# Kernel optimization log

Hardware: AMD Instinct MI355X
Metric: run time of the kernel (lower is better)

## Reference

```python
import jax, jax.numpy as jnp
import numpy as np

H = 1024

def gru_step(x, h, W_ih, W_hh, b_ih, b_hh):
    # torch.nn.GRUCell math; gate order r, z, n
    gi = x @ W_ih.T + b_ih            # [N, 3H]
    gh = h @ W_hh.T + b_hh            # [N, 3H]
    i_r, i_z, i_n = jnp.split(gi, 3, axis=-1)
    h_r, h_z, h_n = jnp.split(gh, 3, axis=-1)
    r = jax.nn.sigmoid(i_r + h_r)
    z = jax.nn.sigmoid(i_z + h_z)
    n = jnp.tanh(i_n + r * h_n)
    return (1.0 - z) * n + z * h


def setup_inputs() -> dict:
    key = jax.random.key(0)
    ks = jax.random.split(key, 12)
    V, Nr, Na = 256, 4096, 4096
    s = 1.0 / np.sqrt(H)
    return {
        'state': jax.random.normal(ks[0], (1, H), jnp.float32),
        'rel_tokens': jax.random.randint(ks[1], (Nr, 3), 0, V, jnp.int32),
        'attr_tokens': jax.random.randint(ks[2], (Na, 2), 0, V, jnp.int32),
        'table': jax.random.normal(ks[3], (V, H), jnp.float32),
        'W_emb': jax.random.normal(ks[4], (H, H), jnp.float32) * s,
        'b_emb': jnp.zeros((H,), jnp.float32),
        'W_ih': jax.random.normal(ks[5], (3 * H, H), jnp.float32) * s,
        'W_hh': jax.random.normal(ks[6], (3 * H, H), jnp.float32) * s,
        'b_ih': jnp.zeros((3 * H,), jnp.float32),
        'b_hh': jnp.zeros((3 * H,), jnp.float32),
        'W1': jax.random.normal(ks[7], (H, H), jnp.float32) * s,
        'b1': jnp.zeros((H,), jnp.float32),
        'W2': jax.random.normal(ks[8], (H, H), jnp.float32) * s,
        'b2': jnp.zeros((H,), jnp.float32),
        'W3': jax.random.normal(ks[9], (1, H), jnp.float32) * s,
        'b3': jnp.zeros((1,), jnp.float32),
        'eps': jax.random.uniform(ks[10], (1,), jnp.float32) * 0.1,
    }


def reference(state, rel_tokens, attr_tokens, table, W_emb, b_emb,
              W_ih, W_hh, b_ih, b_hh, W1, b1, W2, b2, W3, b3, eps):
    Nr, Na = rel_tokens.shape[0], attr_tokens.shape[0]
    # per-clause token embeddings passed through embedding_layer (Linear)
    rel_e = jnp.einsum('nte,he->nth', table[rel_tokens], W_emb) + b_emb   # [Nr,3,H]
    att_e = jnp.einsum('nte,he->nth', table[attr_tokens], W_emb) + b_emb  # [Na,2,H]

    # relation clauses: 3 chained GRU steps from global state
    h = jnp.broadcast_to(state, (Nr, H))
    for t in range(3):
        h = gru_step(rel_e[:, t], h, W_ih, W_hh, b_ih, b_hh)
    rel_h = h
    # attribute clauses: 2 chained GRU steps from global state
    h = jnp.broadcast_to(state, (Na, H))
    for t in range(2):
        h = gru_step(att_e[:, t], h, W_ih, W_hh, b_ih, b_hh)
    attr_h = h

    clause = jnp.concatenate([rel_h, attr_h], axis=0)          # [N, H]
    x = jax.nn.relu(clause @ W1.T + b1)
    x = jax.nn.relu(x @ W2.T + b2)
    logits = (x @ W3.T + b3).reshape(1, -1)                    # [1, N]
    probs = jax.nn.softmax(logits, axis=1)                     # softmax over clauses
    n = jnp.float32(probs.shape[1])
    probs = probs * (1.0 - eps[0]) + eps[0] / n                # eps smoothing
    return probs
```

## Files before the change

kernel.cpp:

```cpp
#include <hip/hip_runtime.h>
#include <math.h>

#define H 1024
#define H3 3072
#define NVOC 256

typedef __attribute__((ext_vector_type(8))) short bf16x8;
typedef __attribute__((ext_vector_type(4))) float f32x4;

__device__ __forceinline__ float sigf(float x) { return 1.0f / (1.0f + expf(-x)); }

__device__ __forceinline__ unsigned short f2bf(float f) {
    unsigned int u = __float_as_uint(f);
    u = (u + 0x7fffu + ((u >> 16) & 1u)) >> 16;
    return (unsigned short)u;
}
__device__ __forceinline__ float bf2f(unsigned short u) {
    return __uint_as_float(((unsigned int)u) << 16);
}

#define MM256(MH, AV, BV)                                                          \
    __builtin_amdgcn_s_setprio(1);                                                 \
    _Pragma("unroll")                                                              \
    for (int m_ = 0; m_ < 4; ++m_)                                                 \
        _Pragma("unroll")                                                          \
        for (int n_ = 0; n_ < 4; ++n_)                                             \
            acc[(MH) * 4 + m_][n_] = __builtin_amdgcn_mfma_f32_16x16x32_bf16(      \
                AV[m_], BV[n_], acc[(MH) * 4 + m_][n_], 0, 0, 0);                  \
    __builtin_amdgcn_s_setprio(0);

#define RDA256(BUF, KQ, MH)                                                        \
    _Pragma("unroll")                                                              \
    for (int m_ = 0; m_ < 4; ++m_)                                                 \
        a[m_] = *reinterpret_cast<const bf16x8*>(                                  \
            ldsb + (BUF) * 65536 + ((KQ) * 2 + (MH)) * 8192 + m_ * 1024 + aoff);

#define RDB256(BUF, KQ, DST)                                                       \
    _Pragma("unroll")                                                              \
    for (int n_ = 0; n_ < 4; ++n_)                                                 \
        DST[n_] = *reinterpret_cast<const bf16x8*>(                                \
            ldsb + (BUF) * 65536 + (KQ) * 16384 + n_ * 1024 + boff);

#define BAR256() __builtin_amdgcn_s_barrier()

template<bool RELU, int OUT_MODE>
__global__ __launch_bounds__(512, 2)
void gemm256(const unsigned short* __restrict__ A, const unsigned short* __restrict__ W,
             const float* __restrict__ bias, void* __restrict__ C,
             int N, int K, int gx,
             const float* __restrict__ w3, float* __restrict__ logits)
{
    __shared__ unsigned short lds[65536];
    char* ldsb = (char*)lds;
    const int tid = threadIdx.x;
    const int wid = tid >> 6, lane = tid & 63;

    const int nwg = gridDim.x;
    const int cpx = nwg >> 3;
    const int bid = blockIdx.x;
    const int swz = (bid & 7) * cpx + (bid >> 3);
    const int bm = (swz / gx) * 256;
    const int bn = (swz % gx) * 256;

    const int g = wid >> 2;
    const int wn = (wid & 3) * 64;
    const int fr = lane & 15, fq = lane >> 4;

    const int aoff = (g * 64 + fr) * 64 + ((fq ^ (fr & 3)) * 16);
    const int boff = (wn + fr) * 64 + ((fq ^ (fr & 3)) * 16) + 32768;

    const int srow = tid >> 2;
    const int scol = ((tid & 3) ^ (srow & 3)) * 8;
    const int arow0 = ((srow >> 6) << 7) + (srow & 63);

    auto stageA = [&](int t, int mh) {
        const int buf = t & 1;
        const unsigned short* src = A + (size_t)(bm + arow0 + mh * 64) * K + t * 64 + scol;
#pragma unroll
        for (int kh = 0; kh < 2; ++kh) {
            char* dst = ldsb + buf * 65536 + (kh * 2 + mh) * 8192 + wid * 1024;
            __builtin_amdgcn_global_load_lds(
                (const __attribute__((address_space(1))) void*)(src + kh * 32),
                (__attribute__((address_space(3))) void*)dst, 16, 0, 0);
        }
    };
    auto stageB = [&](int t, int kh) {
        const int buf = t & 1;
        const unsigned short* src = W + (size_t)(bn + srow) * K + t * 64 + kh * 32 + scol;
#pragma unroll
        for (int j = 0; j < 2; ++j) {
            char* dst = ldsb + buf * 65536 + 32768 + kh * 16384 + j * 8192 + wid * 1024;
            __builtin_amdgcn_global_load_lds(
                (const __attribute__((address_space(1))) void*)(src + (size_t)j * 128 * K),
                (__attribute__((address_space(3))) void*)dst, 16, 0, 0);
        }
    };

    f32x4 acc[8][4];
#pragma unroll
    for (int i = 0; i < 8; i++)
#pragma unroll
        for (int j = 0; j < 4; j++) acc[i][j] = (f32x4){0.f, 0.f, 0.f, 0.f};
    bf16x8 a[4], b0[4], b1[4];

    const int nt = K >> 6;
    const int nIter = nt >> 1;

    stageB(0, 0); stageA(0, 0); stageB(0, 1); stageA(0, 1);
    stageB(1, 0); stageA(1, 0); stageB(1, 1);
    asm volatile("s_waitcnt vmcnt(6)" ::: "memory");
    __builtin_amdgcn_sched_barrier(0);
    BAR256();

    for (int it = 0; it < nIter; ++it) {
        const int t0 = 2 * it;
        const bool full = (it + 1 < nIter);
        RDB256(0, 0, b0); RDA256(0, 0, 0);
        stageA(t0 + 1, 1);
        MM256(0, a, b0); BAR256();
        RDB256(0, 1, b1); RDA256(0, 1, 0);
        if (full) stageB(t0 + 2, 0);
        MM256(0, a, b1); BAR256();
        RDA256(0, 0, 1);
        if (full) stageA(t0 + 2, 0);
        MM256(1, a, b0); BAR256();
        RDA256(0, 1, 1);
        if (full) stageB(t0 + 2, 1);
        MM256(1, a, b1);
        if (full) { asm volatile("s_waitcnt vmcnt(6)" ::: "memory"); }
        else      { asm volatile("s_waitcnt vmcnt(0)" ::: "memory"); }
        __builtin_amdgcn_sched_barrier(0);
        BAR256();
        RDB256(1, 0, b0); RDA256(1, 0, 0);
        if (full) stageA(t0 + 2, 1);
        MM256(0, a, b0); BAR256();
        RDB256(1, 1, b1); RDA256(1, 1, 0);
        if (full) stageB(t0 + 3, 0);
        MM256(0, a, b1); BAR256();
        RDA256(1, 0, 1);
        if (full) stageA(t0 + 3, 0);
        MM256(1, a, b0); BAR256();
        RDA256(1, 1, 1);
        if (full) stageB(t0 + 3, 1);
        MM256(1, a, b1);
        if (full) {
            asm volatile("s_waitcnt vmcnt(6)" ::: "memory");
            __builtin_amdgcn_sched_barrier(0);
        }
        BAR256();
    }

    if (OUT_MODE == 2) {
        float rs[8][4];
#pragma unroll
        for (int m = 0; m < 8; m++)
#pragma unroll
            for (int j = 0; j < 4; j++) rs[m][j] = 0.f;
#pragma unroll
        for (int n = 0; n < 4; n++) {
            const int col = bn + wn + n * 16 + fr;
            const float bv = bias[col];
            const float wv = w3[col];
#pragma unroll
            for (int m = 0; m < 8; m++)
#pragma unroll
                for (int j = 0; j < 4; j++) {
                    float v = acc[m][n][j] + bv;
                    if (RELU) v = fmaxf(v, 0.f);
                    rs[m][j] = fmaf(v, wv, rs[m][j]);
                }
        }
#pragma unroll
        for (int m = 0; m < 8; m++)
#pragma unroll
            for (int j = 0; j < 4; j++) {
                float s = rs[m][j];
                s += __shfl_xor(s, 1); s += __shfl_xor(s, 2);
                s += __shfl_xor(s, 4); s += __shfl_xor(s, 8);
                if (fr == 0) {
                    const int row = bm + g * 128 + (m >> 2) * 64 + (m & 3) * 16 + fq * 4 + j;
                    atomicAdd(logits + row, s);
                }
            }
    } else {
#pragma unroll
        for (int m = 0; m < 8; m++) {
#pragma unroll
            for (int n = 0; n < 4; n++) {
                const int col = bn + wn + n * 16 + fr;
                const float bv = bias[col];
#pragma unroll
                for (int j = 0; j < 4; j++) {
                    const int row = bm + g * 128 + (m >> 2) * 64 + (m & 3) * 16 + fq * 4 + j;
                    float v = acc[m][n][j] + bv;
                    if (RELU) v = fmaxf(v, 0.f);
                    ((unsigned short*)C)[(size_t)row * N + col] = f2bf(v);
                }
            }
        }
    }
}

template<bool RELU, int OUT_MODE>
__global__ __launch_bounds__(256)
void gemm_bf16(const unsigned short* __restrict__ A, const unsigned short* __restrict__ W,
               const float* __restrict__ bias, void* __restrict__ C,
               int N, int K, int gx, int Kc,
               const float* __restrict__ w3, float* __restrict__ logits)
{
    __shared__ unsigned short As[4][128 * 32];
    __shared__ unsigned short Ws[4][128 * 32];
    const int tid = threadIdx.x;
    const int wid = tid >> 6, lane = tid & 63;

    const int nwg = gridDim.x;
    const int cpx = nwg >> 3;
    const int bid = blockIdx.x;
    const int swz = (bid & 7) * cpx + (bid >> 3);
    const int bm = (swz / gx) * 128;
    const int bn = (swz % gx) * 128;
    const int k_base = blockIdx.y * Kc;
    const int nt = Kc >> 5;

    const int wm = (wid >> 1) * 64, wn = (wid & 1) * 64;
    const int fr = lane & 15;
    const int fq = lane >> 4;
    const int perm = fq ^ (fr & 3);

    f32x4 acc[4][4];
#pragma unroll
    for (int i = 0; i < 4; i++)
#pragma unroll
        for (int j = 0; j < 4; j++) acc[i][j] = (f32x4){0.f, 0.f, 0.f, 0.f};

    const int srow = tid >> 2;
    const int schunk = (tid & 3) ^ (srow & 3);
    const unsigned short* aS = A + (size_t)(bm + srow) * K + k_base + schunk * 8;
    const unsigned short* wS = W + (size_t)(bn + srow) * K + k_base + schunk * 8;
    const size_t rstep = (size_t)64 * K;

    auto stage = [&](int b, int t) {
        const unsigned short* a0 = aS + t * 32;
        const unsigned short* w0 = wS + t * 32;
        __builtin_amdgcn_global_load_lds(
            (const __attribute__((address_space(1))) void*)a0,
            (__attribute__((address_space(3))) void*)(&As[b][wid * 512]), 16, 0, 0);
        __builtin_amdgcn_global_load_lds(
            (const __attribute__((address_space(1))) void*)(a0 + rstep),
            (__attribute__((address_space(3))) void*)(&As[b][2048 + wid * 512]), 16, 0, 0);
        __builtin_amdgcn_global_load_lds(
            (const __attribute__((address_space(1))) void*)w0,
            (__attribute__((address_space(3))) void*)(&Ws[b][wid * 512]), 16, 0, 0);
        __builtin_amdgcn_global_load_lds(
            (const __attribute__((address_space(1))) void*)(w0 + rstep),
            (__attribute__((address_space(3))) void*)(&Ws[b][2048 + wid * 512]), 16, 0, 0);
    };

    stage(0, 0);
    if (nt > 1) stage(1, 1);
    if (nt > 2) stage(2, 2);

    for (int t = 0; t < nt; ++t) {
        if (t + 2 < nt)      asm volatile("s_waitcnt vmcnt(8)" ::: "memory");
        else if (t + 1 < nt) asm volatile("s_waitcnt vmcnt(4)" ::: "memory");
        else                 asm volatile("s_waitcnt vmcnt(0)" ::: "memory");
        __builtin_amdgcn_s_barrier();
        __builtin_amdgcn_sched_barrier(0);
        if (t + 3 < nt) stage((t + 3) & 3, t + 3);

        const unsigned short* as = &As[t & 3][0];
        const unsigned short* ws = &Ws[t & 3][0];
        bf16x8 a[4], b[4];
#pragma unroll
        for (int m = 0; m < 4; m++)
            a[m] = *reinterpret_cast<const bf16x8*>(as + (wm + m * 16 + fr) * 32 + perm * 8);
#pragma unroll
        for (int n = 0; n < 4; n++)
            b[n] = *reinterpret_cast<const bf16x8*>(ws + (wn + n * 16 + fr) * 32 + perm * 8);
        __builtin_amdgcn_s_setprio(1);
#pragma unroll
        for (int m = 0; m < 4; m++)
#pragma unroll
            for (int n = 0; n < 4; n++)
                acc[m][n] = __builtin_amdgcn_mfma_f32_16x16x32_bf16(a[m], b[n], acc[m][n], 0, 0, 0);
        __builtin_amdgcn_s_setprio(0);
    }

    if (OUT_MODE == 3) {
        float* Cf = (float*)C;
#pragma unroll
        for (int m = 0; m < 4; m++)
#pragma unroll
            for (int n = 0; n < 4; n++) {
                const int col = bn + wn + n * 16 + fr;
#pragma unroll
                for (int j = 0; j < 4; j++) {
                    const int row = bm + wm + m * 16 + fq * 4 + j;
                    atomicAdd(Cf + (size_t)row * N + col, acc[m][n][j]);
                }
            }
    } else {
#pragma unroll
        for (int m = 0; m < 4; m++) {
#pragma unroll
            for (int n = 0; n < 4; n++) {
                const int col = bn + wn + n * 16 + fr;
                const float bv = bias[col];
#pragma unroll
                for (int j = 0; j < 4; j++) {
                    const int row = bm + wm + m * 16 + fq * 4 + j;
                    float v = acc[m][n][j] + bv;
                    if (RELU) v = fmaxf(v, 0.f);
                    if (OUT_MODE == 1)
                        ((unsigned short*)C)[(size_t)row * N + col] = f2bf(v);
                    else
                        ((float*)C)[(size_t)row * N + col] = v;
                }
            }
        }
    }
}

__global__ void cvt_all(const float* __restrict__ W_hh, const float* __restrict__ W_ih,
                        const float* __restrict__ W1, const float* __restrict__ W2,
                        const float* __restrict__ W_emb, const float* __restrict__ table,
                        unsigned short* __restrict__ W_hhb, unsigned short* __restrict__ W_ihb,
                        unsigned short* __restrict__ W1b, unsigned short* __restrict__ W2b,
                        unsigned short* __restrict__ W_embb, unsigned short* __restrict__ tableb)
{
    const int C1 = H3 * H, C2 = H * H, C3 = NVOC * H;
    int off = (blockIdx.x * blockDim.x + threadIdx.x) * 4;
    const float* src; unsigned short* dst;
    if (off < C1)               { src = W_hh;  dst = W_hhb; }
    else if ((off -= C1) < C1)  { src = W_ih;  dst = W_ihb; }
    else if ((off -= C1) < C2)  { src = W1;    dst = W1b; }
    else if ((off -= C2) < C2)  { src = W2;    dst = W2b; }
    else if ((off -= C2) < C2)  { src = W_emb; dst = W_embb; }
    else if ((off -= C2) < C3)  { src = table; dst = tableb; }
    else return;
    float4 v = *reinterpret_cast<const float4*>(src + off);
    ushort4 o;
    o.x = f2bf(v.x); o.y = f2bf(v.y); o.z = f2bf(v.z); o.w = f2bf(v.w);
    *reinterpret_cast<ushort4*>(dst + off) = o;
}

__global__ void prefill(const float* __restrict__ b_emb, const float* __restrict__ b_ih,
                        const float* __restrict__ b_hh,
                        float* __restrict__ emb32, float* __restrict__ Gi,
                        float* __restrict__ gh1, float* __restrict__ logits, int Ntot)
{
    const int E = NVOC * H, G = NVOC * H3;
    int i = blockIdx.x * blockDim.x + threadIdx.x;
    if (i < E)                { emb32[i] = b_emb[i & (H - 1)]; return; }
    if ((i -= E) < G)         { Gi[i] = b_ih[i % H3]; return; }
    if ((i -= G) < G)         { gh1[i] = b_hh[i % H3]; return; }
    if ((i -= G) < Ntot)      logits[i] = 0.f;
}

__global__ void cvt_emb(const float* __restrict__ in, unsigned short* __restrict__ out)
{
    int i = (blockIdx.x * blockDim.x + threadIdx.x) * 4;
    float4 v = *reinterpret_cast<const float4*>(in + i);
    ushort4 o;
    o.x = f2bf(v.x); o.y = f2bf(v.y); o.z = f2bf(v.z); o.w = f2bf(v.w);
    *reinterpret_cast<ushort4*>(out + i) = o;
}

__global__ void gemv_bf16w(const float* __restrict__ x, const unsigned short* __restrict__ Wm,
                           const float* __restrict__ bias, float* __restrict__ out,
                           int N, int K)
{
    int wid = threadIdx.x >> 6;
    int lane = threadIdx.x & 63;
    int n = blockIdx.x * (blockDim.x >> 6) + wid;
    if (n >= N) return;
    const unsigned short* wr = Wm + (size_t)n * K;
    float s = 0.f;
    for (int p = 0; p < K; p += 256) {
        float4 xv = *reinterpret_cast<const float4*>(x + p + lane * 4);
        ushort4 wv = *reinterpret_cast<const ushort4*>(wr + p + lane * 4);
        s = fmaf(xv.x, bf2f(wv.x), s); s = fmaf(xv.y, bf2f(wv.y), s);
        s = fmaf(xv.z, bf2f(wv.z), s); s = fmaf(xv.w, bf2f(wv.w), s);
    }
#pragma unroll
    for (int off = 32; off; off >>= 1) s += __shfl_down(s, off);
    if (lane == 0) out[n] = s + (bias ? bias[n] : 0.f);
}

__global__ void h1_combine(const float* __restrict__ Gi, const float* __restrict__ gh0,
                           const float* __restrict__ state, float* __restrict__ h1,
                           unsigned short* __restrict__ h1b)
{
    int idx = blockIdx.x * blockDim.x + threadIdx.x;
    int v = idx >> 10, h = idx & (H - 1);
    const float* g = Gi + (size_t)v * H3;
    float r = sigf(g[h] + gh0[h]);
    float z = sigf(g[H + h] + gh0[H + h]);
    float n = tanhf(fmaf(r, gh0[2 * H + h], g[2 * H + h]));
    float v2 = (1.f - z) * n + z * state[h];
    h1[idx] = v2;
    h1b[idx] = f2bf(v2);
}

__global__ void step2_both(const int* __restrict__ rel, const int* __restrict__ attr, int Nr,
                           const float* __restrict__ Gi, const float* __restrict__ gh1,
                           const float* __restrict__ h1,
                           unsigned short* __restrict__ h2b, unsigned short* __restrict__ attr_out)
{
    int idx = blockIdx.x * blockDim.x + threadIdx.x;
    int row = idx >> 10, h = idx & (H - 1);
    int t0, t1, orow = row;
    unsigned short* dst;
    if (row < Nr) { t0 = rel[row * 3 + 0]; t1 = rel[row * 3 + 1]; dst = h2b; }
    else { orow = row - Nr; t0 = attr[orow * 2 + 0]; t1 = attr[orow * 2 + 1]; dst = attr_out; }
    const float* g = Gi + (size_t)t1 * H3;
    const float* gh = gh1 + (size_t)t0 * H3;
    float r = sigf(g[h] + gh[h]);
    float z = sigf(g[H + h] + gh[H + h]);
    float n = tanhf(fmaf(r, gh[2 * H + h], g[2 * H + h]));
    float v = (1.f - z) * n + z * h1[(size_t)t0 * H + h];
    dst[(size_t)orow * H + h] = f2bf(v);
}

__global__ void step3_rel(const int* __restrict__ toks,
                          const float* __restrict__ Gi, const unsigned short* __restrict__ gh2b,
                          const unsigned short* __restrict__ h2b, unsigned short* __restrict__ outb)
{
    int idx = blockIdx.x * blockDim.x + threadIdx.x;
    int row = idx >> 10, h = idx & (H - 1);
    int t2 = toks[row * 3 + 2];
    const float* g = Gi + (size_t)t2 * H3;
    const unsigned short* gh = gh2b + (size_t)row * H3;
    float r = sigf(g[h] + bf2f(gh[h]));
    float z = sigf(g[H + h] + bf2f(gh[H + h]));
    float n = tanhf(fmaf(r, bf2f(gh[2 * H + h]), g[2 * H + h]));
    outb[idx] = f2bf((1.f - z) * n + z * bf2f(h2b[idx]));
}

__global__ void softmax_eps(const float* __restrict__ logits, const float* __restrict__ epsp,
                            float* __restrict__ out, int N)
{
    __shared__ float smax[16], ssum[16];
    int tid = threadIdx.x;
    int nw = blockDim.x >> 6;
    float m = -INFINITY;
    for (int i = tid; i < N; i += blockDim.x) m = fmaxf(m, logits[i]);
#pragma unroll
    for (int off = 32; off; off >>= 1) m = fmaxf(m, __shfl_down(m, off));
    if ((tid & 63) == 0) smax[tid >> 6] = m;
    __syncthreads();
    float M = smax[0];
    for (int i = 1; i < nw; i++) M = fmaxf(M, smax[i]);
    float s = 0.f;
    for (int i = tid; i < N; i += blockDim.x) s += expf(logits[i] - M);
#pragma unroll
    for (int off = 32; off; off >>= 1) s += __shfl_down(s, off);
    if ((tid & 63) == 0) ssum[tid >> 6] = s;
    __syncthreads();
    float S = 0.f;
    for (int i = 0; i < nw; i++) S += ssum[i];
    float e = epsp[0];
    float mul = (1.f - e) / S;
    float add = e / (float)N;
    for (int i = tid; i < N; i += blockDim.x) out[i] = expf(logits[i] - M) * mul + add;
}

extern "C" void kernel_launch(void* const* d_in, const int* in_sizes, int n_in,
                              void* d_out, int out_size, void* d_ws, size_t ws_size,
                              hipStream_t stream)
{
    const float* state       = (const float*)d_in[0];
    const int*   rel_tokens  = (const int*)d_in[1];
    const int*   attr_tokens = (const int*)d_in[2];
    const float* table       = (const float*)d_in[3];
    const float* W_emb       = (const float*)d_in[4];
    const float* b_emb       = (const float*)d_in[5];
    const float* W_ih        = (const float*)d_in[6];
    const float* W_hh        = (const float*)d_in[7];
    const float* b_ih        = (const float*)d_in[8];
    const float* b_hh        = (const float*)d_in[9];
    const float* W1          = (const float*)d_in[10];
    const float* b1          = (const float*)d_in[11];
    const float* W2          = (const float*)d_in[12];
    const float* b2          = (const float*)d_in[13];
    const float* W3          = (const float*)d_in[14];
    const float* eps         = (const float*)d_in[16];

    const int Nr = in_sizes[1] / 3;
    const int Na = in_sizes[2] / 2;
    const int Ntot = Nr + Na;

    float* ws     = (float*)d_ws;
    float* Gi     = ws;
    float* gh0    = Gi + NVOC * H3;
    float* h1     = gh0 + H3;
    float* gh1    = h1 + NVOC * H;
    float* emb32  = gh1 + NVOC * H3;
    float* logits = emb32 + NVOC * H;
    unsigned short* W_hhb   = (unsigned short*)(logits + Ntot);
    unsigned short* W_ihb   = W_hhb + (size_t)H3 * H;
    unsigned short* W1b     = W_ihb + (size_t)H3 * H;
    unsigned short* W2b     = W1b + (size_t)H * H;
    unsigned short* W_embb  = W2b + (size_t)H * H;
    unsigned short* tableb  = W_embb + (size_t)H * H;
    unsigned short* embb    = tableb + (size_t)NVOC * H;
    unsigned short* h1b     = embb + (size_t)NVOC * H;
    unsigned short* h2b     = h1b + (size_t)NVOC * H;
    unsigned short* gh2b    = h2b + (size_t)Nr * H;
    unsigned short* clauseb = gh2b + (size_t)Nr * H3;
    unsigned short* x1b     = clauseb + (size_t)Ntot * H;

    {
        const int total = 2 * H3 * H + 3 * H * H + NVOC * H;
        cvt_all<<<(total / 4 + 255) / 256, 256, 0, stream>>>(
            W_hh, W_ih, W1, W2, W_emb, table,
            W_hhb, W_ihb, W1b, W2b, W_embb, tableb);
        const int pf = NVOC * H + 2 * NVOC * H3 + Ntot;
        prefill<<<(pf + 255) / 256, 256, 0, stream>>>(b_emb, b_ih, b_hh,
                                                      emb32, Gi, gh1, logits, Ntot);
    }

    gemm_bf16<false, 3><<<dim3((H / 128) * (NVOC / 128), 4), 256, 0, stream>>>(
        tableb, W_embb, nullptr, emb32, H, H, H / 128, H / 4, nullptr, nullptr);
    cvt_emb<<<NVOC * H / 4 / 256, 256, 0, stream>>>(emb32, embb);
    gemm_bf16<false, 3><<<dim3((H3 / 128) * (NVOC / 128), 4), 256, 0, stream>>>(
        embb, W_ihb, nullptr, Gi, H3, H, H3 / 128, H / 4, nullptr, nullptr);
    gemv_bf16w<<<H3 / 4, 256, 0, stream>>>(state, W_hhb, b_hh, gh0, H3, H);
    h1_combine<<<NVOC * H / 256, 256, 0, stream>>>(Gi, gh0, state, h1, h1b);
    gemm_bf16<false, 3><<<dim3((H3 / 128) * (NVOC / 128), 4), 256, 0, stream>>>(
        h1b, W_hhb, nullptr, gh1, H3, H, H3 / 128, H / 4, nullptr, nullptr);
    step2_both<<<Ntot * (H / 256), 256, 0, stream>>>(rel_tokens, attr_tokens, Nr,
                                                     Gi, gh1, h1, h2b,
                                                     clauseb + (size_t)Nr * H);
    gemm256<false, 1><<<(Nr / 256) * (H3 / 256), 512, 0, stream>>>(
        h2b, W_hhb, b_hh, gh2b, H3, H, H3 / 256, nullptr, nullptr);
    step3_rel<<<Nr * (H / 256), 256, 0, stream>>>(rel_tokens, Gi, gh2b, h2b, clauseb);
    gemm256<true, 1><<<(Ntot / 256) * (H / 256), 512, 0, stream>>>(
        clauseb, W1b, b1, x1b, H, H, H / 256, nullptr, nullptr);
    gemm256<true, 2><<<(Ntot / 256) * (H / 256), 512, 0, stream>>>(
        x1b, W2b, b2, nullptr, H, H, H / 256, W3, logits);
    softmax_eps<<<1, 1024, 0, stream>>>(logits, eps, (float*)d_out, Ntot);
}
```

Measured before the change: 311.7 us.

## Fuse weight conversion, bias prefill and state GEMV into one prep kernel; restage LDS

The separate weight-conversion, bias-prefill and state·W_hh GEMV kernels are merged into a single prep kernel. It computes gh0 in fp32 straight from the fp32 W_hh rows while converting them, which removes two launches and a re-read of W_hh. The 256x256 GEMM's LDS staging is also reorganized: each thread loads one 16-byte chunk per 64-row unit, rows are 128 bytes with an 8-way XOR swizzle, and the K-loop is a single-tile loop in place of the manually unrolled two-tile loop. These changes alter the bank-conflict pattern and the vmcnt accounting, so the prefetch schedule could stall differently or become incorrect.

```diff
diff --git a/kernel.cpp b/kernel.cpp
--- a/kernel.cpp
+++ b/kernel.cpp
@@ -29,17 +29,19 @@
                 AV[m_], BV[n_], acc[(MH) * 4 + m_][n_], 0, 0, 0);                  \
     __builtin_amdgcn_s_setprio(0);
 
-#define RDA256(BUF, KQ, MH)                                                        \
+#define RDA256(BUF, MH, KQ)                                                        \
     _Pragma("unroll")                                                              \
     for (int m_ = 0; m_ < 4; ++m_)                                                 \
         a[m_] = *reinterpret_cast<const bf16x8*>(                                  \
-            ldsb + (BUF) * 65536 + ((KQ) * 2 + (MH)) * 8192 + m_ * 1024 + aoff);
+            ldsb + (BUF) * 65536 + (g * 128 + (MH) * 64 + m_ * 16 + fr) * 128 +    \
+            (((KQ) * 4 + fq) ^ (fr & 7)) * 16);
 
 #define RDB256(BUF, KQ, DST)                                                       \
     _Pragma("unroll")                                                              \
     for (int n_ = 0; n_ < 4; ++n_)                                                 \
         DST[n_] = *reinterpret_cast<const bf16x8*>(                                \
-            ldsb + (BUF) * 65536 + (KQ) * 16384 + n_ * 1024 + boff);
+            ldsb + (BUF) * 65536 + 32768 + (wn + n_ * 16 + fr) * 128 +             \
+            (((KQ) * 4 + fq) ^ (fr & 7)) * 16);
 
 #define BAR256() __builtin_amdgcn_s_barrier()
 
@@ -66,34 +68,16 @@
     const int wn = (wid & 3) * 64;
     const int fr = lane & 15, fq = lane >> 4;
 
-    const int aoff = (g * 64 + fr) * 64 + ((fq ^ (fr & 3)) * 16);
-    const int boff = (wn + fr) * 64 + ((fq ^ (fr & 3)) * 16) + 32768;
-
-    const int srow = tid >> 2;
-    const int scol = ((tid & 3) ^ (srow & 3)) * 8;
-    const int arow0 = ((srow >> 6) << 7) + (srow & 63);
-
-    auto stageA = [&](int t, int mh) {
-        const int buf = t & 1;
-        const unsigned short* src = A + (size_t)(bm + arow0 + mh * 64) * K + t * 64 + scol;
-#pragma unroll
-        for (int kh = 0; kh < 2; ++kh) {
-            char* dst = ldsb + buf * 65536 + (kh * 2 + mh) * 8192 + wid * 1024;
-            __builtin_amdgcn_global_load_lds(
-                (const __attribute__((address_space(1))) void*)(src + kh * 32),
-                (__attribute__((address_space(3))) void*)dst, 16, 0, 0);
-        }
-    };
-    auto stageB = [&](int t, int kh) {
-        const int buf = t & 1;
-        const unsigned short* src = W + (size_t)(bn + srow) * K + t * 64 + kh * 32 + scol;
-#pragma unroll
-        for (int j = 0; j < 2; ++j) {
-            char* dst = ldsb + buf * 65536 + 32768 + kh * 16384 + j * 8192 + wid * 1024;
-            __builtin_amdgcn_global_load_lds(
-                (const __attribute__((address_space(1))) void*)(src + (size_t)j * 128 * K),
-                (__attribute__((address_space(3))) void*)dst, 16, 0, 0);
-        }
+    const int sr = tid >> 3;
+    const int sc = ((tid & 7) ^ (sr & 7)) * 8;
+    auto stage_unit = [&](int t, int u) {
+        const unsigned short* src = (u < 4)
+            ? A + (size_t)(bm + u * 64 + sr) * K + t * 64 + sc
+            : W + (size_t)(bn + (u - 4) * 64 + sr) * K + t * 64 + sc;
+        char* dst = ldsb + (t & 1) * 65536 + u * 8192 + tid * 16;
+        __builtin_amdgcn_global_load_lds(
+            (const __attribute__((address_space(1))) void*)src,
+            (__attribute__((address_space(3))) void*)dst, 16, 0, 0);
     };
 
     f32x4 acc[8][4];
@@ -104,47 +88,34 @@
     bf16x8 a[4], b0[4], b1[4];
 
     const int nt = K >> 6;
-    const int nIter = nt >> 1;
-
-    stageB(0, 0); stageA(0, 0); stageB(0, 1); stageA(0, 1);
-    stageB(1, 0); stageA(1, 0); stageB(1, 1);
+
+#pragma unroll
+    for (int u = 0; u < 8; ++u) stage_unit(0, u);
+    stage_unit(1, 0); stage_unit(1, 2); stage_unit(1, 4);
+    stage_unit(1, 5); stage_unit(1, 6); stage_unit(1, 7);
     asm volatile("s_waitcnt vmcnt(6)" ::: "memory");
     __builtin_amdgcn_sched_barrier(0);
     BAR256();
 
-    for (int it = 0; it < nIter; ++it) {
-        const int t0 = 2 * it;
-        const bool full = (it + 1 < nIter);
-        RDB256(0, 0, b0); RDA256(0, 0, 0);
-        stageA(t0 + 1, 1);
+    for (int t = 0; t < nt; ++t) {
+        const int buf = t & 1;
+        RDB256(buf, 0, b0); RDA256(buf, 0, 0);
+        if (t + 1 < nt) stage_unit(t + 1, 1);
         MM256(0, a, b0); BAR256();
-        RDB256(0, 1, b1); RDA256(0, 1, 0);
-        if (full) stageB(t0 + 2, 0);
+        RDB256(buf, 1, b1); RDA256(buf, 0, 1);
+        if (t + 1 < nt) stage_unit(t + 1, 3);
         MM256(0, a, b1); BAR256();
-        RDA256(0, 0, 1);
-        if (full) stageA(t0 + 2, 0);
+        RDA256(buf, 1, 0);
+        if (t + 2 < nt) { stage_unit(t + 2, 0); stage_unit(t + 2, 2); stage_unit(t + 2, 4); }
         MM256(1, a, b0); BAR256();
-        RDA256(0, 1, 1);
-        if (full) stageB(t0 + 2, 1);
+        RDA256(buf, 1, 1);
+        if (t + 2 < nt) { stage_unit(t + 2, 5); stage_unit(t + 2, 6); stage_unit(t + 2, 7); }
         MM256(1, a, b1);
-        if (full) { asm volatile("s_waitcnt vmcnt(6)" ::: "memory"); }
-        else      { asm volatile("s_waitcnt vmcnt(0)" ::: "memory"); }
-        __builtin_amdgcn_sched_barrier(0);
-        BAR256();
-        RDB256(1, 0, b0); RDA256(1, 0, 0);
-        if (full) stageA(t0 + 2, 1);
-        MM256(0, a, b0); BAR256();
-        RDB256(1, 1, b1); RDA256(1, 1, 0);
-        if (full) stageB(t0 + 3, 0);
-        MM256(0, a, b1); BAR256();
-        RDA256(1, 0, 1);
-        if (full) stageA(t0 + 3, 0);
-        MM256(1, a, b0); BAR256();
-        RDA256(1, 1, 1);
-        if (full) stageB(t0 + 3, 1);
-        MM256(1, a, b1);
-        if (full) {
+        if (t + 2 < nt) {
             asm volatile("s_waitcnt vmcnt(6)" ::: "memory");
+            __builtin_amdgcn_sched_barrier(0);
+        } else if (t + 1 < nt) {
+            asm volatile("s_waitcnt vmcnt(0)" ::: "memory");
             __builtin_amdgcn_sched_barrier(0);
         }
         BAR256();
@@ -321,40 +292,66 @@
     }
 }
 
-__global__ void cvt_all(const float* __restrict__ W_hh, const float* __restrict__ W_ih,
-                        const float* __restrict__ W1, const float* __restrict__ W2,
-                        const float* __restrict__ W_emb, const float* __restrict__ table,
-                        unsigned short* __restrict__ W_hhb, unsigned short* __restrict__ W_ihb,
-                        unsigned short* __restrict__ W1b, unsigned short* __restrict__ W2b,
-                        unsigned short* __restrict__ W_embb, unsigned short* __restrict__ tableb)
-{
-    const int C1 = H3 * H, C2 = H * H, C3 = NVOC * H;
-    int off = (blockIdx.x * blockDim.x + threadIdx.x) * 4;
-    const float* src; unsigned short* dst;
-    if (off < C1)               { src = W_hh;  dst = W_hhb; }
-    else if ((off -= C1) < C1)  { src = W_ih;  dst = W_ihb; }
-    else if ((off -= C1) < C2)  { src = W1;    dst = W1b; }
-    else if ((off -= C2) < C2)  { src = W2;    dst = W2b; }
-    else if ((off -= C2) < C2)  { src = W_emb; dst = W_embb; }
-    else if ((off -= C2) < C3)  { src = table; dst = tableb; }
-    else return;
+__global__ __launch_bounds__(256)
+void prep(const float* __restrict__ W_hh, const float* __restrict__ W_ih,
+          const float* __restrict__ W1, const float* __restrict__ W2,
+          const float* __restrict__ W_emb, const float* __restrict__ table,
+          const float* __restrict__ state, const float* __restrict__ b_emb,
+          const float* __restrict__ b_ih, const float* __restrict__ b_hh,
+          unsigned short* __restrict__ W_hhb, unsigned short* __restrict__ W_ihb,
+          unsigned short* __restrict__ W1b, unsigned short* __restrict__ W2b,
+          unsigned short* __restrict__ W_embb, unsigned short* __restrict__ tableb,
+          float* __restrict__ gh0, float* __restrict__ emb32, float* __restrict__ Gi,
+          float* __restrict__ gh1, float* __restrict__ logits)
+{
+    int b = blockIdx.x;
+    const int t = threadIdx.x;
+    if (b < 3072) {
+        float4 w = *reinterpret_cast<const float4*>(W_hh + (size_t)b * H + t * 4);
+        ushort4 o; o.x = f2bf(w.x); o.y = f2bf(w.y); o.z = f2bf(w.z); o.w = f2bf(w.w);
+        *reinterpret_cast<ushort4*>(W_hhb + (size_t)b * H + t * 4) = o;
+        float4 sv = *reinterpret_cast<const float4*>(state + t * 4);
+        float s = w.x * sv.x + w.y * sv.y + w.z * sv.z + w.w * sv.w;
+#pragma unroll
+        for (int off = 32; off; off >>= 1) s += __shfl_down(s, off);
+        __shared__ float ps[4];
+        if ((t & 63) == 0) ps[t >> 6] = s;
+        __syncthreads();
+        if (t == 0) gh0[b] = ps[0] + ps[1] + ps[2] + ps[3] + b_hh[b];
+        return;
+    }
+    b -= 3072;
+    const float* src = nullptr; unsigned short* dst = nullptr;
+    if (b < 3072)      { src = W_ih;  dst = W_ihb; }
+    else if ((b -= 3072) < 1024) { src = W1; dst = W1b; }
+    else if ((b -= 1024) < 1024) { src = W2; dst = W2b; }
+    else if ((b -= 1024) < 1024) { src = W_emb; dst = W_embb; }
+    else if ((b -= 1024) < 256)  { src = table; dst = tableb; }
+    else {
+        b -= 256;
+        if (b < 256) {
+            int i = b * 1024 + t * 4;
+            *reinterpret_cast<float4*>(emb32 + i) =
+                *reinterpret_cast<const float4*>(b_emb + (i & (H - 1)));
+        } else if ((b -= 256) < 768) {
+            int i = b * 1024 + t * 4;
+            *reinterpret_cast<float4*>(Gi + i) =
+                *reinterpret_cast<const float4*>(b_ih + i % H3);
+        } else if ((b -= 768) < 768) {
+            int i = b * 1024 + t * 4;
+            *reinterpret_cast<float4*>(gh1 + i) =
+                *reinterpret_cast<const float4*>(b_hh + i % H3);
+        } else {
+            b -= 768;
+            int i = b * 1024 + t * 4;
+            *reinterpret_cast<float4*>(logits + i) = (float4){0.f, 0.f, 0.f, 0.f};
+        }
+        return;
+    }
+    const int off = b * 1024 + t * 4;
     float4 v = *reinterpret_cast<const float4*>(src + off);
-    ushort4 o;
-    o.x = f2bf(v.x); o.y = f2bf(v.y); o.z = f2bf(v.z); o.w = f2bf(v.w);
+    ushort4 o; o.x = f2bf(v.x); o.y = f2bf(v.y); o.z = f2bf(v.z); o.w = f2bf(v.w);
     *reinterpret_cast<ushort4*>(dst + off) = o;
-}
-
-__global__ void prefill(const float* __restrict__ b_emb, const float* __restrict__ b_ih,
-                        const float* __restrict__ b_hh,
-                        float* __restrict__ emb32, float* __restrict__ Gi,
-                        float* __restrict__ gh1, float* __restrict__ logits, int Ntot)
-{
-    const int E = NVOC * H, G = NVOC * H3;
-    int i = blockIdx.x * blockDim.x + threadIdx.x;
-    if (i < E)                { emb32[i] = b_emb[i & (H - 1)]; return; }
-    if ((i -= E) < G)         { Gi[i] = b_ih[i % H3]; return; }
-    if ((i -= G) < G)         { gh1[i] = b_hh[i % H3]; return; }
-    if ((i -= G) < Ntot)      logits[i] = 0.f;
 }
 
 __global__ void cvt_emb(const float* __restrict__ in, unsigned short* __restrict__ out)
@@ -364,27 +361,6 @@
     ushort4 o;
     o.x = f2bf(v.x); o.y = f2bf(v.y); o.z = f2bf(v.z); o.w = f2bf(v.w);
     *reinterpret_cast<ushort4*>(out + i) = o;
-}
-
-__global__ void gemv_bf16w(const float* __restrict__ x, const unsigned short* __restrict__ Wm,
-                           const float* __restrict__ bias, float* __restrict__ out,
-                           int N, int K)
-{
-    int wid = threadIdx.x >> 6;
-    int lane = threadIdx.x & 63;
-    int n = blockIdx.x * (blockDim.x >> 6) + wid;
-    if (n >= N) return;
-    const unsigned short* wr = Wm + (size_t)n * K;
-    float s = 0.f;
-    for (int p = 0; p < K; p += 256) {
-        float4 xv = *reinterpret_cast<const float4*>(x + p + lane * 4);
-        ushort4 wv = *reinterpret_cast<const ushort4*>(wr + p + lane * 4);
-        s = fmaf(xv.x, bf2f(wv.x), s); s = fmaf(xv.y, bf2f(wv.y), s);
-        s = fmaf(xv.z, bf2f(wv.z), s); s = fmaf(xv.w, bf2f(wv.w), s);
-    }
-#pragma unroll
-    for (int off = 32; off; off >>= 1) s += __shfl_down(s, off);
-    if (lane == 0) out[n] = s + (bias ? bias[n] : 0.f);
 }
 
 __global__ void h1_combine(const float* __restrict__ Gi, const float* __restrict__ gh0,
@@ -510,22 +486,16 @@
     unsigned short* clauseb = gh2b + (size_t)Nr * H3;
     unsigned short* x1b     = clauseb + (size_t)Ntot * H;
 
-    {
-        const int total = 2 * H3 * H + 3 * H * H + NVOC * H;
-        cvt_all<<<(total / 4 + 255) / 256, 256, 0, stream>>>(
-            W_hh, W_ih, W1, W2, W_emb, table,
-            W_hhb, W_ihb, W1b, W2b, W_embb, tableb);
-        const int pf = NVOC * H + 2 * NVOC * H3 + Ntot;
-        prefill<<<(pf + 255) / 256, 256, 0, stream>>>(b_emb, b_ih, b_hh,
-                                                      emb32, Gi, gh1, logits, Ntot);
-    }
+    prep<<<11272, 256, 0, stream>>>(W_hh, W_ih, W1, W2, W_emb, table, state,
+                                    b_emb, b_ih, b_hh,
+                                    W_hhb, W_ihb, W1b, W2b, W_embb, tableb,
+                                    gh0, emb32, Gi, gh1, logits);
 
     gemm_bf16<false, 3><<<dim3((H / 128) * (NVOC / 128), 4), 256, 0, stream>>>(
         tableb, W_embb, nullptr, emb32, H, H, H / 128, H / 4, nullptr, nullptr);
     cvt_emb<<<NVOC * H / 4 / 256, 256, 0, stream>>>(emb32, embb);
     gemm_bf16<false, 3><<<dim3((H3 / 128) * (NVOC / 128), 4), 256, 0, stream>>>(
         embb, W_ihb, nullptr, Gi, H3, H, H3 / 128, H / 4, nullptr, nullptr);
-    gemv_bf16w<<<H3 / 4, 256, 0, stream>>>(state, W_hhb, b_hh, gh0, H3, H);
     h1_combine<<<NVOC * H / 256, 256, 0, stream>>>(Gi, gh0, state, h1, h1b);
     gemm_bf16<false, 3><<<dim3((H3 / 128) * (NVOC / 128), 4), 256, 0, stream>>>(
         h1b, W_hhb, nullptr, gh1, H3, H, H3 / 128, H / 4, nullptr, nullptr);
```

New measurement: 303.5 us. -2.6%, faster.
